# Kernel optimization log

Hardware: AMD Instinct MI355X
Metric: run time of the kernel (lower is better)

The kernel has to match this reference:

```python
import jax, jax.numpy as jnp
import numpy as np

D_MODEL = 1024
N_HEADS = 16
HEAD_DIM = D_MODEL // N_HEADS
THETA = 10000.0
B, S = 4, 2048


def setup_inputs() -> dict:
    key = jax.random.key(0)
    ks = jax.random.split(key, 5)
    scale = 1.0 / np.sqrt(D_MODEL)
    x = jax.random.normal(ks[0], (B, S, D_MODEL), dtype=jnp.float32)
    token_positions = jnp.broadcast_to(jnp.arange(S, dtype=jnp.int32)[None, :], (B, S))
    WQ = jax.random.normal(ks[1], (D_MODEL, D_MODEL), dtype=jnp.float32) * scale
    WK = jax.random.normal(ks[2], (D_MODEL, D_MODEL), dtype=jnp.float32) * scale
    WV = jax.random.normal(ks[3], (D_MODEL, D_MODEL), dtype=jnp.float32) * scale
    WO = jax.random.normal(ks[4], (D_MODEL, D_MODEL), dtype=jnp.float32) * scale
    return {"x": x, "token_positions": token_positions, "WQ": WQ, "WK": WK, "WV": WV, "WO": WO}


def _apply_rope(t, token_positions):
    # t: [b, h, s, d]; token_positions: [b, s]
    d = t.shape[-1]
    inv_freq = THETA ** (-jnp.arange(0, d, 2, dtype=jnp.float32) / d)  # [d/2]
    ang = token_positions.astype(jnp.float32)[:, None, :, None] * inv_freq  # [b,1,s,d/2]
    cos, sin = jnp.cos(ang), jnp.sin(ang)
    t_even, t_odd = t[..., 0::2], t[..., 1::2]
    r_even = t_even * cos - t_odd * sin
    r_odd = t_even * sin + t_odd * cos
    out = jnp.stack([r_even, r_odd], axis=-1)  # interleave pairs back
    return out.reshape(t.shape)


def reference(x, token_positions, WQ, WK, WV, WO):
    b, s, _ = x.shape
    def proj(W):
        y = jnp.einsum('bsd,ed->bse', x, W)  # Linear: x @ W^T, W is [out,in]
        return y.reshape(b, s, N_HEADS, HEAD_DIM).transpose(0, 2, 1, 3)  # [b,h,s,d]
    Q = _apply_rope(proj(WQ), token_positions)
    K = _apply_rope(proj(WK), token_positions)
    V = proj(WV)
    scores = jnp.einsum('bhqd,bhkd->bhqk', Q, K) / jnp.sqrt(jnp.float32(HEAD_DIM))
    causal = jnp.tril(jnp.ones((s, s), dtype=bool))
    scores = jnp.where(causal, scores, -jnp.inf)
    attn = jax.nn.softmax(scores, axis=-1)
    out = jnp.einsum('bhqk,bhkd->bhqd', attn, V)
    out = out.transpose(0, 2, 1, 3).reshape(b, s, D_MODEL)
    return jnp.einsum('bse,oe->bso', out, WO)
```

## Files before the change

### kernel.cpp

```cpp
#include <hip/hip_runtime.h>

typedef __bf16 bf16x8 __attribute__((ext_vector_type(8)));
typedef __bf16 bf16x2 __attribute__((ext_vector_type(2)));
typedef float f32x4 __attribute__((ext_vector_type(4)));
typedef unsigned short u16;
typedef unsigned int u32;

#define MFMA16(a, b, c) __builtin_amdgcn_mfma_f32_16x16x32_bf16((a), (b), (c), 0, 0, 0)

__device__ __forceinline__ u16 f2b(float f) {
  u32 u = __float_as_uint(f);
  u += 0x7FFFu + ((u >> 16) & 1u);
  return (u16)(u >> 16);
}
__device__ __forceinline__ float b2f(u16 h) { return __uint_as_float(((u32)h) << 16); }

__device__ __forceinline__ u32 pkbf(float a, float b) {
  bf16x2 h = {(__bf16)a, (__bf16)b};
  return __builtin_bit_cast(u32, h);
}

__device__ __forceinline__ float exp2_(float x) {
#if __has_builtin(__builtin_amdgcn_exp2f)
  return __builtin_amdgcn_exp2f(x);
#else
  return exp2f(x);
#endif
}

__device__ __forceinline__ void glds16(const void* g, void* l) {
  __builtin_amdgcn_global_load_lds((const __attribute__((address_space(1))) void*)g,
                                   (__attribute__((address_space(3))) void*)l, 16, 0, 0);
}

__global__ __launch_bounds__(256) void cvt_k(const float* __restrict__ x,
                                             const float* __restrict__ wq,
                                             const float* __restrict__ wk,
                                             const float* __restrict__ wv,
                                             const float* __restrict__ wo,
                                             u16* __restrict__ dst) {
  size_t e = ((size_t)blockIdx.x * 256 + threadIdx.x) * 4;
  const float* src;
  size_t off;
  if (e < 8388608ull) {
    src = x; off = e;
  } else {
    size_t r = e - 8388608ull;
    u32 wi = (u32)(r >> 20);
    off = r & 1048575ull;
    src = (wi == 0) ? wq : (wi == 1) ? wk : (wi == 2) ? wv : wo;
  }
  float4 v = *(const float4*)(src + off);
  ushort4 o = make_ushort4(f2b(v.x), f2b(v.y), f2b(v.z), f2b(v.w));
  *(ushort4*)(dst + e) = o;
}

__global__ __launch_bounds__(256) void rope_tab_k(const int* __restrict__ pos,
                                                  float2* __restrict__ tab) {
  int i = blockIdx.x * 256 + threadIdx.x;
  int row = i >> 5, j = i & 31;
  float p = (float)pos[row];
  float inv = exp2f((float)j * -0.41524101186092029f);
  float s, c;
  sincosf(p * inv, &s, &c);
  tab[i] = make_float2(c, s);
}

__global__ __launch_bounds__(256) void gemm_qkv_k(const u16* __restrict__ Xb,
                                                  const u16* __restrict__ Wq,
                                                  const u16* __restrict__ Wk,
                                                  const u16* __restrict__ Wv,
                                                  const float2* __restrict__ tab,
                                                  u16* __restrict__ Qp,
                                                  u16* __restrict__ Kp,
                                                  u16* __restrict__ Vt) {
  __shared__ u16 As[128 * 32];
  __shared__ u16 Bs[128 * 32];
  const int wgid = blockIdx.x;
  const int xcd = wgid & 7;
  const int idx = wgid >> 3;
  const int panel = xcd * 24 + (idx >> 3);
  const int nt = idx & 7;
  const int z = panel >> 6;
  const int mt = panel & 63;
  const u16* W = (z == 0) ? Wq : (z == 1) ? Wk : Wv;
  const int tid = threadIdx.x, wave = tid >> 6, lane = tid & 63;
  const int wr = (wave >> 1) * 64, wc = (wave & 1) * 64;
  const int lr = lane & 15, lg = lane >> 4;

  const size_t arow = (size_t)(mt * 128 + wave * 32 + (lane >> 2)) * 1024 + (lane & 3) * 8;
  const size_t brow = (size_t)(nt * 128 + wave * 32 + (lane >> 2)) * 1024 + (lane & 3) * 8;
  u16* Ad0 = &As[(wave * 32) * 32];
  u16* Ad1 = &As[(wave * 32 + 16) * 32];
  u16* Bd0 = &Bs[(wave * 32) * 32];
  u16* Bd1 = &Bs[(wave * 32 + 16) * 32];

  f32x4 acc[4][4];
#pragma unroll
  for (int i = 0; i < 4; ++i)
#pragma unroll
    for (int j = 0; j < 4; ++j) acc[i][j] = (f32x4){0.f, 0.f, 0.f, 0.f};

  for (int kt = 0; kt < 1024; kt += 32) {
    glds16(Xb + arow + kt, Ad0);
    glds16(Xb + arow + kt + 16 * 1024, Ad1);
    glds16(W + brow + kt, Bd0);
    glds16(W + brow + kt + 16 * 1024, Bd1);
    __syncthreads();
    bf16x8 af[4], bfr[4];
#pragma unroll
    for (int mi = 0; mi < 4; ++mi)
      af[mi] = *(const bf16x8*)&As[(wr + mi * 16 + lr) * 32 + lg * 8];
#pragma unroll
    for (int ni = 0; ni < 4; ++ni)
      bfr[ni] = *(const bf16x8*)&Bs[(wc + ni * 16 + lr) * 32 + lg * 8];
#pragma unroll
    for (int mi = 0; mi < 4; ++mi)
#pragma unroll
      for (int ni = 0; ni < 4; ++ni)
        acc[mi][ni] = MFMA16(af[mi], bfr[ni], acc[mi][ni]);
    __syncthreads();
  }

  if (z < 2) {
    u16* out = (z == 0) ? Qp : Kp;
    const float scl = (z == 0) ? 0.18033688011112043f : 1.0f;
#pragma unroll
    for (int mi = 0; mi < 4; ++mi)
#pragma unroll
      for (int ni = 0; ni < 4; ++ni) {
        int row0 = mt * 128 + wr + mi * 16 + lg * 4;
        int col = nt * 128 + wc + ni * 16 + lr;
        int j = (col >> 1) & 31;
        float sgn = (col & 1) ? 1.f : -1.f;
#pragma unroll
        for (int r = 0; r < 4; ++r) {
          float self = acc[mi][ni][r];
          float partner = __shfl_xor(self, 1);
          float2 cs = tab[(size_t)(row0 + r) * 32 + j];
          float o = (self * cs.x + partner * cs.y * sgn) * scl;
          out[(size_t)(row0 + r) * 1024 + col] = f2b(o);
        }
      }
  } else {
#pragma unroll
    for (int mi = 0; mi < 4; ++mi)
#pragma unroll
      for (int ni = 0; ni < 4; ++ni) {
        int row0 = mt * 128 + wr + mi * 16 + lg * 4;
        int e = nt * 128 + wc + ni * 16 + lr;
        int b = row0 >> 11, s = row0 & 2047;
        ushort4 pk = make_ushort4(f2b(acc[mi][ni][0]), f2b(acc[mi][ni][1]),
                                  f2b(acc[mi][ni][2]), f2b(acc[mi][ni][3]));
        *(ushort4*)&Vt[((size_t)(b * 1024 + e)) * 2048 + s] = pk;
      }
  }
}

__global__ __launch_bounds__(256) void fattn_k(const u16* __restrict__ Qp,
                                               const u16* __restrict__ Kp,
                                               const u16* __restrict__ Vt,
                                               u16* __restrict__ Ao) {
  __shared__ u16 Ks[2][64 * 64];
  __shared__ u16 Vs[2][64 * 64];
  __shared__ u16 Ps[4][32 * 64];
  const int blk = blockIdx.x;
  const int g = blk & 7, jj = blk >> 3;
  const int bh = g * 8 + (jj & 7);
  const int qt = 15 - (jj >> 3);
  const int b = bh >> 4, h = bh & 15;
  const int tid = threadIdx.x, wave = tid >> 6, lane = tid & 63;
  const int lr = lane & 15, lg = lane >> 4;
  const int q0w = qt * 128 + wave * 32;

  bf16x8 qf[2][2];
#pragma unroll
  for (int qh = 0; qh < 2; ++qh) {
    const u16* qb = Qp + ((size_t)(b * 2048 + q0w + qh * 16 + lr)) * 1024 + h * 64 + lg * 8;
    qf[qh][0] = *(const bf16x8*)qb;
    qf[qh][1] = *(const bf16x8*)(qb + 32);
  }

  float m[2], l[2];
  f32x4 oacc[2][4];
#pragma unroll
  for (int qh = 0; qh < 2; ++qh) {
    m[qh] = -1e30f; l[qh] = 0.f;
#pragma unroll
    for (int d4 = 0; d4 < 4; ++d4) oacc[qh][d4] = (f32x4){0.f, 0.f, 0.f, 0.f};
  }

  const int srow = lane >> 3;
  const int schunk = (lane & 7) ^ srow;
  const u16* kbase = Kp + ((size_t)(b * 2048 + 16 * wave + srow)) * 1024 + h * 64 + schunk * 8;
  const u16* vbase = Vt + ((size_t)(b * 1024 + h * 64 + 16 * wave + srow)) * 2048 + schunk * 8;
  char* psbase = (char*)&Ps[wave][0];

  const int ktmax = 2 * qt + 1;
  const int ktmask = q0w >> 6;
  const int ktneed = 2 * qt + (wave >> 1);

  glds16(kbase, &Ks[0][(16 * wave) * 64]);
  glds16(kbase + 8192, &Ks[0][(16 * wave + 8) * 64]);
  glds16(vbase, &Vs[0][(16 * wave) * 64]);
  glds16(vbase + 16384, &Vs[0][(16 * wave + 8) * 64]);

  int cur = 0;
  for (int kt = 0; kt <= ktmax; ++kt, cur ^= 1) {
    __syncthreads();
    if (kt < ktmax) {
      const int nx = cur ^ 1, k1 = kt + 1;
      glds16(kbase + (size_t)k1 * 65536, &Ks[nx][(16 * wave) * 64]);
      glds16(kbase + (size_t)k1 * 65536 + 8192, &Ks[nx][(16 * wave + 8) * 64]);
      glds16(vbase + k1 * 64, &Vs[nx][(16 * wave) * 64]);
      glds16(vbase + k1 * 64 + 16384, &Vs[nx][(16 * wave + 8) * 64]);
    }
    if (kt > ktneed) continue;
    const u16* KB = &Ks[cur][0];
    const u16* VB = &Vs[cur][0];

    f32x4 sc[2][4];
#pragma unroll
    for (int ks = 0; ks < 4; ++ks) {
      const int krow = ks * 16 + lr;
      const int sw = lr & 7;
      bf16x8 kf0 = *(const bf16x8*)&KB[krow * 64 + ((lg ^ sw) * 8)];
      bf16x8 kf1 = *(const bf16x8*)&KB[krow * 64 + (((lg + 4) ^ sw) * 8)];
#pragma unroll
      for (int qh = 0; qh < 2; ++qh) {
        f32x4 s = (f32x4){0.f, 0.f, 0.f, 0.f};
        s = MFMA16(kf0, qf[qh][0], s);
        s = MFMA16(kf1, qf[qh][1], s);
        sc[qh][ks] = s;
      }
    }
    if (kt >= ktmask) {
#pragma unroll
      for (int qh = 0; qh < 2; ++qh) {
        int q = q0w + qh * 16 + lr;
#pragma unroll
        for (int ks = 0; ks < 4; ++ks)
#pragma unroll
          for (int r = 0; r < 4; ++r) {
            int kv = kt * 64 + ks * 16 + lg * 4 + r;
            if (kv > q) sc[qh][ks][r] = -__builtin_inff();
          }
      }
    }

#pragma unroll
    for (int qh = 0; qh < 2; ++qh) {
      float pm = sc[qh][0][0];
#pragma unroll
      for (int ks = 0; ks < 4; ++ks)
#pragma unroll
        for (int r = 0; r < 4; ++r) pm = fmaxf(pm, sc[qh][ks][r]);
      pm = fmaxf(pm, __shfl_xor(pm, 16));
      pm = fmaxf(pm, __shfl_xor(pm, 32));
      if (__any(pm > m[qh] + 8.f)) {
        float mn = fmaxf(m[qh], pm);
        float corr = exp2_(m[qh] - mn);
        m[qh] = mn;
        l[qh] *= corr;
        float cb[4];
#pragma unroll
        for (int r = 0; r < 4; ++r) cb[r] = __shfl(corr, (lane & 48) | (lg * 4 + r));
#pragma unroll
        for (int d4 = 0; d4 < 4; ++d4)
#pragma unroll
          for (int r = 0; r < 4; ++r) oacc[qh][d4][r] *= cb[r];
      }
      float rs = 0.f;
#pragma unroll
      for (int ks = 0; ks < 4; ++ks)
#pragma unroll
        for (int r = 0; r < 4; ++r) {
          float p = exp2_(sc[qh][ks][r] - m[qh]);
          sc[qh][ks][r] = p;
          rs += p;
        }
      rs += __shfl_xor(rs, 16);
      rs += __shfl_xor(rs, 32);
      l[qh] += rs;
    }

#pragma unroll
    for (int qh = 0; qh < 2; ++qh) {
      const int row = qh * 16 + lr;
      const int sw = lr & 7;
#pragma unroll
      for (int ks = 0; ks < 4; ++ks) {
        const int chunk = (2 * ks + (lg >> 1)) ^ sw;
        char* p = psbase + row * 128 + chunk * 16 + (lg & 1) * 8;
        *(uint2*)p = make_uint2(pkbf(sc[qh][ks][0], sc[qh][ks][1]),
                                pkbf(sc[qh][ks][2], sc[qh][ks][3]));
      }
    }
    bf16x8 pa[2][2];
#pragma unroll
    for (int qh = 0; qh < 2; ++qh) {
      const int row = qh * 16 + lr;
      const int sw = lr & 7;
      pa[qh][0] = *(const bf16x8*)(psbase + row * 128 + ((lg ^ sw) * 16));
      pa[qh][1] = *(const bf16x8*)(psbase + row * 128 + (((lg + 4) ^ sw) * 16));
    }
#pragma unroll
    for (int d4 = 0; d4 < 4; ++d4) {
      const int vrow = d4 * 16 + lr;
      const int sw = lr & 7;
      bf16x8 vf0 = *(const bf16x8*)&VB[vrow * 64 + ((lg ^ sw) * 8)];
      bf16x8 vf1 = *(const bf16x8*)&VB[vrow * 64 + (((lg + 4) ^ sw) * 8)];
      oacc[0][d4] = MFMA16(pa[0][0], vf0, oacc[0][d4]);
      oacc[0][d4] = MFMA16(pa[0][1], vf1, oacc[0][d4]);
      oacc[1][d4] = MFMA16(pa[1][0], vf0, oacc[1][d4]);
      oacc[1][d4] = MFMA16(pa[1][1], vf1, oacc[1][d4]);
    }
  }

#pragma unroll
  for (int qh = 0; qh < 2; ++qh) {
    float lb[4];
#pragma unroll
    for (int r = 0; r < 4; ++r) lb[r] = __shfl(l[qh], (lane & 48) | (lg * 4 + r));
#pragma unroll
    for (int r = 0; r < 4; ++r) {
      float inv = 1.f / lb[r];
      int q = q0w + qh * 16 + lg * 4 + r;
      u16* orow = Ao + ((size_t)(b * 2048 + q)) * 1024 + h * 64 + lr;
#pragma unroll
      for (int d4 = 0; d4 < 4; ++d4) orow[d4 * 16] = f2b(oacc[qh][d4][r] * inv);
    }
  }
}

__global__ __launch_bounds__(256) void gemm_wo_k(const u16* __restrict__ Ab,
                                                 const u16* __restrict__ Wo,
                                                 float* __restrict__ Out) {
  __shared__ u16 As[128 * 32];
  __shared__ u16 Bs[128 * 32];
  const int wgid = blockIdx.x;
  const int xcd = wgid & 7;
  const int idx = wgid >> 3;
  const int mt = xcd * 8 + (idx >> 3);
  const int nt = idx & 7;
  const int tid = threadIdx.x, wave = tid >> 6, lane = tid & 63;
  const int wr = (wave >> 1) * 64, wc = (wave & 1) * 64;
  const int lr = lane & 15, lg = lane >> 4;
  const size_t arow = (size_t)(mt * 128 + wave * 32 + (lane >> 2)) * 1024 + (lane & 3) * 8;
  const size_t brow = (size_t)(nt * 128 + wave * 32 + (lane >> 2)) * 1024 + (lane & 3) * 8;
  u16* Ad0 = &As[(wave * 32) * 32];
  u16* Ad1 = &As[(wave * 32 + 16) * 32];
  u16* Bd0 = &Bs[(wave * 32) * 32];
  u16* Bd1 = &Bs[(wave * 32 + 16) * 32];

  f32x4 acc[4][4];
#pragma unroll
  for (int i = 0; i < 4; ++i)
#pragma unroll
    for (int j = 0; j < 4; ++j) acc[i][j] = (f32x4){0.f, 0.f, 0.f, 0.f};

  for (int kt = 0; kt < 1024; kt += 32) {
    glds16(Ab + arow + kt, Ad0);
    glds16(Ab + arow + kt + 16 * 1024, Ad1);
    glds16(Wo + brow + kt, Bd0);
    glds16(Wo + brow + kt + 16 * 1024, Bd1);
    __syncthreads();
    bf16x8 af[4], bfr[4];
#pragma unroll
    for (int mi = 0; mi < 4; ++mi)
      af[mi] = *(const bf16x8*)&As[(wr + mi * 16 + lr) * 32 + lg * 8];
#pragma unroll
    for (int ni = 0; ni < 4; ++ni)
      bfr[ni] = *(const bf16x8*)&Bs[(wc + ni * 16 + lr) * 32 + lg * 8];
#pragma unroll
    for (int mi = 0; mi < 4; ++mi)
#pragma unroll
      for (int ni = 0; ni < 4; ++ni)
        acc[mi][ni] = MFMA16(af[mi], bfr[ni], acc[mi][ni]);
    __syncthreads();
  }
#pragma unroll
  for (int mi = 0; mi < 4; ++mi)
#pragma unroll
    for (int ni = 0; ni < 4; ++ni) {
      int row0 = mt * 128 + wr + mi * 16 + lg * 4;
      int col = nt * 128 + wc + ni * 16 + lr;
#pragma unroll
      for (int r = 0; r < 4; ++r)
        Out[(size_t)(row0 + r) * 1024 + col] = acc[mi][ni][r];
    }
}

extern "C" void kernel_launch(void* const* d_in, const int* in_sizes, int n_in,
                              void* d_out, int out_size, void* d_ws, size_t ws_size,
                              hipStream_t stream) {
  const float* x = (const float*)d_in[0];
  const int* pos = (const int*)d_in[1];
  const float* wq = (const float*)d_in[2];
  const float* wk = (const float*)d_in[3];
  const float* wv = (const float*)d_in[4];
  const float* wo = (const float*)d_in[5];

  char* ws = (char*)d_ws;
  u16* xb = (u16*)ws;
  u16* wqb = xb + 8388608;
  u16* wkb = wqb + 1048576;
  u16* wvb = wkb + 1048576;
  u16* wob = wvb + 1048576;
  float2* tab = (float2*)(ws + 25165824);
  u16* Qp = (u16*)(ws + 27262976);
  u16* Kp = (u16*)(ws + 27262976 + 16777216);
  u16* Vt = (u16*)(ws + 27262976 + 2 * 16777216);
  u16* Ao = (u16*)(ws + 27262976 + 3 * 16777216);

  hipLaunchKernelGGL(cvt_k, dim3(12288), dim3(256), 0, stream, x, wq, wk, wv, wo, xb);
  hipLaunchKernelGGL(rope_tab_k, dim3(1024), dim3(256), 0, stream, pos, tab);
  hipLaunchKernelGGL(gemm_qkv_k, dim3(1536), dim3(256), 0, stream, xb, wqb, wkb, wvb,
                     tab, Qp, Kp, Vt);
  hipLaunchKernelGGL(fattn_k, dim3(1024), dim3(256), 0, stream, Qp, Kp, Vt, Ao);
  hipLaunchKernelGGL(gemm_wo_k, dim3(512), dim3(256), 0, stream, Ao, wob, (float*)d_out);
}
```

Before: 199.0 us.

## Enlarge QKV GEMM tiles to 256x256 with 4-stage LDS pipeline and swizzle

Rewrites the QKV projection GEMM to use 256x256 tiles with 512 threads, a 4-deep ring of shared-memory buffers fed by async global-to-LDS loads, and an XOR swizzle on the K offset to avoid bank conflicts. The main loop is split into two half-steps that interleave loads, barriers and MFMA bursts under raised wave priority. The goal is to raise arithmetic intensity and hide global load latency behind MFMA work. The cost is more registers and LDS per block and fewer blocks (384) on the device, which can hurt occupancy and tail balance.

```diff
diff --git a/kernel.cpp b/kernel.cpp
--- a/kernel.cpp
+++ b/kernel.cpp
@@ -66,76 +66,121 @@
   tab[i] = make_float2(c, s);
 }
 
-__global__ __launch_bounds__(256) void gemm_qkv_k(const u16* __restrict__ Xb,
-                                                  const u16* __restrict__ Wq,
-                                                  const u16* __restrict__ Wk,
-                                                  const u16* __restrict__ Wv,
-                                                  const float2* __restrict__ tab,
-                                                  u16* __restrict__ Qp,
-                                                  u16* __restrict__ Kp,
-                                                  u16* __restrict__ Vt) {
-  __shared__ u16 As[128 * 32];
-  __shared__ u16 Bs[128 * 32];
+__global__ __launch_bounds__(512, 2) void gemm_qkv_k(const u16* __restrict__ Xb,
+                                                     const u16* __restrict__ Wq,
+                                                     const u16* __restrict__ Wk,
+                                                     const u16* __restrict__ Wv,
+                                                     const float2* __restrict__ tab,
+                                                     u16* __restrict__ Qp,
+                                                     u16* __restrict__ Kp,
+                                                     u16* __restrict__ Vt) {
+  __shared__ u16 As[4][8192];
+  __shared__ u16 Bs[4][8192];
   const int wgid = blockIdx.x;
   const int xcd = wgid & 7;
   const int idx = wgid >> 3;
-  const int panel = xcd * 24 + (idx >> 3);
-  const int nt = idx & 7;
-  const int z = panel >> 6;
-  const int mt = panel & 63;
+  const int P = xcd * 12 + (idx >> 2);
+  const int nt = idx & 3;
+  const int z = P >> 5;
+  const int mt = P & 31;
   const u16* W = (z == 0) ? Wq : (z == 1) ? Wk : Wv;
-  const int tid = threadIdx.x, wave = tid >> 6, lane = tid & 63;
-  const int wr = (wave >> 1) * 64, wc = (wave & 1) * 64;
+  const int t = threadIdx.x;
+  const int wave = t >> 6, lane = t & 63;
   const int lr = lane & 15, lg = lane >> 4;
-
-  const size_t arow = (size_t)(mt * 128 + wave * 32 + (lane >> 2)) * 1024 + (lane & 3) * 8;
-  const size_t brow = (size_t)(nt * 128 + wave * 32 + (lane >> 2)) * 1024 + (lane & 3) * 8;
-  u16* Ad0 = &As[(wave * 32) * 32];
-  u16* Ad1 = &As[(wave * 32 + 16) * 32];
-  u16* Bd0 = &Bs[(wave * 32) * 32];
-  u16* Bd1 = &Bs[(wave * 32 + 16) * 32];
-
-  f32x4 acc[4][4];
-#pragma unroll
-  for (int i = 0; i < 4; ++i)
+  const int wr = wave >> 2, wc = wave & 3;
+  const int swz4 = (lr & 3) ^ ((lr >> 2) & 3);
+  const int koff = (lg ^ swz4) * 8;
+
+  const int ct = (t & 3) ^ ((t >> 2) & 3) ^ ((t >> 4) & 3);
+  const int r0 = t >> 2;
+  const u16* a0 = Xb + (size_t)(mt * 256 + r0) * 1024 + ct * 8;
+  const u16* a1 = a0 + 128 * 1024;
+  const u16* b0 = W + (size_t)(nt * 256 + r0) * 1024 + ct * 8;
+  const u16* b1 = b0 + 128 * 1024;
+  const int d0 = t * 8, d1 = 4096 + t * 8;
+
+  f32x4 acc[8][4];
+#pragma unroll
+  for (int i = 0; i < 8; ++i)
 #pragma unroll
     for (int j = 0; j < 4; ++j) acc[i][j] = (f32x4){0.f, 0.f, 0.f, 0.f};
 
-  for (int kt = 0; kt < 1024; kt += 32) {
-    glds16(Xb + arow + kt, Ad0);
-    glds16(Xb + arow + kt + 16 * 1024, Ad1);
-    glds16(W + brow + kt, Bd0);
-    glds16(W + brow + kt + 16 * 1024, Bd1);
-    __syncthreads();
-    bf16x8 af[4], bfr[4];
-#pragma unroll
-    for (int mi = 0; mi < 4; ++mi)
-      af[mi] = *(const bf16x8*)&As[(wr + mi * 16 + lr) * 32 + lg * 8];
-#pragma unroll
-    for (int ni = 0; ni < 4; ++ni)
-      bfr[ni] = *(const bf16x8*)&Bs[(wc + ni * 16 + lr) * 32 + lg * 8];
-#pragma unroll
-    for (int mi = 0; mi < 4; ++mi)
-#pragma unroll
-      for (int ni = 0; ni < 4; ++ni)
-        acc[mi][ni] = MFMA16(af[mi], bfr[ni], acc[mi][ni]);
-    __syncthreads();
+#pragma unroll
+  for (int tt = 0; tt < 3; ++tt) {
+    glds16(a0 + tt * 32, &As[tt][d0]);
+    glds16(a1 + tt * 32, &As[tt][d1]);
+    glds16(b0 + tt * 32, &Bs[tt][d0]);
+    glds16(b1 + tt * 32, &Bs[tt][d1]);
+  }
+  asm volatile("s_waitcnt vmcnt(8)" ::: "memory");
+  __builtin_amdgcn_s_barrier();
+
+  const int arb = (wr * 128 + lr) * 32 + koff;
+  const int brb = (wc * 64 + lr) * 32 + koff;
+
+  for (int tau = 0; tau < 32; ++tau) {
+    const u16* Asl = &As[tau & 3][0];
+    const u16* Bsl = &Bs[tau & 3][0];
+    u16* Adst = &As[(tau + 3) & 3][0];
+    u16* Bdst = &Bs[(tau + 3) & 3][0];
+    const int kg = (tau + 3) * 32;
+    bf16x8 af[8], bq0, bq1;
+#pragma unroll
+    for (int mi = 0; mi < 8; ++mi) af[mi] = *(const bf16x8*)&Asl[arb + mi * 512];
+    bq0 = *(const bf16x8*)&Bsl[brb];
+    bq1 = *(const bf16x8*)&Bsl[brb + 512];
+    if (tau < 29) { glds16(a0 + kg, &Adst[d0]); glds16(a1 + kg, &Adst[d1]); }
+    __builtin_amdgcn_s_barrier();
+    asm volatile("s_waitcnt lgkmcnt(0)" ::: "memory");
+    __builtin_amdgcn_sched_barrier(0);
+    __builtin_amdgcn_s_setprio(1);
+#pragma unroll
+    for (int mi = 0; mi < 8; ++mi) {
+      acc[mi][0] = MFMA16(af[mi], bq0, acc[mi][0]);
+      acc[mi][1] = MFMA16(af[mi], bq1, acc[mi][1]);
+    }
+    __builtin_amdgcn_s_setprio(0);
+    __builtin_amdgcn_sched_barrier(0);
+    if (tau < 29) asm volatile("s_waitcnt vmcnt(8)" ::: "memory");
+    else if (tau == 29) asm volatile("s_waitcnt vmcnt(4)" ::: "memory");
+    else asm volatile("s_waitcnt vmcnt(0)" ::: "memory");
+    __builtin_amdgcn_s_barrier();
+    bq0 = *(const bf16x8*)&Bsl[brb + 1024];
+    bq1 = *(const bf16x8*)&Bsl[brb + 1536];
+    if (tau < 29) { glds16(b0 + kg, &Bdst[d0]); glds16(b1 + kg, &Bdst[d1]); }
+    __builtin_amdgcn_s_barrier();
+    asm volatile("s_waitcnt lgkmcnt(0)" ::: "memory");
+    __builtin_amdgcn_sched_barrier(0);
+    __builtin_amdgcn_s_setprio(1);
+#pragma unroll
+    for (int mi = 0; mi < 8; ++mi) {
+      acc[mi][2] = MFMA16(af[mi], bq0, acc[mi][2]);
+      acc[mi][3] = MFMA16(af[mi], bq1, acc[mi][3]);
+    }
+    __builtin_amdgcn_s_setprio(0);
+    __builtin_amdgcn_sched_barrier(0);
+    if (tau < 29) asm volatile("s_waitcnt vmcnt(8)" ::: "memory");
+    else if (tau == 29) asm volatile("s_waitcnt vmcnt(4)" ::: "memory");
+    else asm volatile("s_waitcnt vmcnt(0)" ::: "memory");
+    __builtin_amdgcn_s_barrier();
   }
 
   if (z < 2) {
     u16* out = (z == 0) ? Qp : Kp;
     const float scl = (z == 0) ? 0.18033688011112043f : 1.0f;
-#pragma unroll
-    for (int mi = 0; mi < 4; ++mi)
-#pragma unroll
-      for (int ni = 0; ni < 4; ++ni) {
-        int row0 = mt * 128 + wr + mi * 16 + lg * 4;
-        int col = nt * 128 + wc + ni * 16 + lr;
+    const int rbase = mt * 256 + wr * 128 + lg * 4;
+    const int cbase = nt * 256 + wc * 64 + lr;
+#pragma unroll
+    for (int mi = 0; mi < 8; ++mi)
+#pragma unroll
+      for (int nj = 0; nj < 4; ++nj) {
+        int row0 = rbase + mi * 16;
+        int col = cbase + nj * 16;
         int j = (col >> 1) & 31;
         float sgn = (col & 1) ? 1.f : -1.f;
 #pragma unroll
         for (int r = 0; r < 4; ++r) {
-          float self = acc[mi][ni][r];
+          float self = acc[mi][nj][r];
           float partner = __shfl_xor(self, 1);
           float2 cs = tab[(size_t)(row0 + r) * 32 + j];
           float o = (self * cs.x + partner * cs.y * sgn) * scl;
@@ -143,15 +188,17 @@
         }
       }
   } else {
-#pragma unroll
-    for (int mi = 0; mi < 4; ++mi)
-#pragma unroll
-      for (int ni = 0; ni < 4; ++ni) {
-        int row0 = mt * 128 + wr + mi * 16 + lg * 4;
-        int e = nt * 128 + wc + ni * 16 + lr;
+    const int rbase = mt * 256 + wr * 128 + lg * 4;
+    const int cbase = nt * 256 + wc * 64 + lr;
+#pragma unroll
+    for (int mi = 0; mi < 8; ++mi)
+#pragma unroll
+      for (int nj = 0; nj < 4; ++nj) {
+        int row0 = rbase + mi * 16;
+        int e = cbase + nj * 16;
         int b = row0 >> 11, s = row0 & 2047;
-        ushort4 pk = make_ushort4(f2b(acc[mi][ni][0]), f2b(acc[mi][ni][1]),
-                                  f2b(acc[mi][ni][2]), f2b(acc[mi][ni][3]));
+        ushort4 pk = make_ushort4(f2b(acc[mi][nj][0]), f2b(acc[mi][nj][1]),
+                                  f2b(acc[mi][nj][2]), f2b(acc[mi][nj][3]));
         *(ushort4*)&Vt[((size_t)(b * 1024 + e)) * 2048 + s] = pk;
       }
   }
@@ -415,7 +462,7 @@
 
   hipLaunchKernelGGL(cvt_k, dim3(12288), dim3(256), 0, stream, x, wq, wk, wv, wo, xb);
   hipLaunchKernelGGL(rope_tab_k, dim3(1024), dim3(256), 0, stream, pos, tab);
-  hipLaunchKernelGGL(gemm_qkv_k, dim3(1536), dim3(256), 0, stream, xb, wqb, wkb, wvb,
+  hipLaunchKernelGGL(gemm_qkv_k, dim3(384), dim3(512), 0, stream, xb, wqb, wkb, wvb,
                      tab, Qp, Kp, Vt);
   hipLaunchKernelGGL(fattn_k, dim3(1024), dim3(256), 0, stream, Qp, Kp, Vt, Ao);
   hipLaunchKernelGGL(gemm_wo_k, dim3(512), dim3(256), 0, stream, Ao, wob, (float*)d_out);
```

Result: slower. 206.4 us (+3.7%).
